# Kernel optimization log

Hardware: AMD Instinct MI355X
Metric: run time of the kernel (lower is better)

Reference implementation:

```python
import jax, jax.numpy as jnp
import numpy as np

N = 100000   # nodes
E = 1000000  # edges
F_IN = 128
H = 256
G = 64       # graphs in batch
EPS = 1e-5   # BatchNorm eps


def setup_inputs() -> dict:
    key = jax.random.key(0)
    ks = jax.random.split(key, 16)
    s = 0.05
    d = {}
    d["x"] = jax.random.normal(ks[0], (N, F_IN), jnp.float32)
    d["edge_index"] = jax.random.randint(ks[1], (2, E), 0, N, dtype=jnp.int32)
    d["batch"] = jnp.sort(jax.random.randint(ks[2], (N,), 0, G, dtype=jnp.int32))
    # block1 (128 -> 256, has projection)
    d["W1"] = jax.random.normal(ks[3], (F_IN, H), jnp.float32) * s
    d["b1"] = jnp.zeros((H,), jnp.float32)
    d["g1"] = jnp.ones((H,), jnp.float32)
    d["be1"] = jnp.zeros((H,), jnp.float32)
    d["P1"] = jax.random.normal(ks[4], (F_IN, H), jnp.float32) * s
    # blocks 2-4 (256 -> 256)
    for i, k in zip((2, 3, 4), (ks[5], ks[6], ks[7])):
        d[f"W{i}"] = jax.random.normal(k, (H, H), jnp.float32) * s
        d[f"b{i}"] = jnp.zeros((H,), jnp.float32)
        d[f"g{i}"] = jnp.ones((H,), jnp.float32)
        d[f"be{i}"] = jnp.zeros((H,), jnp.float32)
    d["Wl"] = jax.random.normal(ks[8], (H, 1), jnp.float32) * s
    d["bl"] = jnp.zeros((1,), jnp.float32)
    return d


def _gcn_norm(edge_index):
    # PyG gcn_norm: add self-loops, deg from dst column, norm = d^-1/2[src]*d^-1/2[dst]
    src, dst = edge_index[0], edge_index[1]
    deg = jax.ops.segment_sum(jnp.ones((E,), jnp.float32), dst, num_segments=N) + 1.0
    dis = jax.lax.rsqrt(deg)
    enorm = dis[src] * dis[dst]          # [E] normalization per edge
    self_w = 1.0 / deg                   # self-loop weight = deg^-1
    return src, dst, enorm, self_w


def _block(x, src, dst, enorm, self_w, W, b, g, be, P=None):
    hw = x @ W                                            # [N, H]
    msg = hw[src] * enorm[:, None]                        # [E, H] gather
    agg = jax.ops.segment_sum(msg, dst, num_segments=N)   # scatter-add
    agg = agg + hw * self_w[:, None] + b                  # self-loop + bias
    # BatchNorm1d (training-mode batch statistics, biased variance)
    m = jnp.mean(agg, axis=0)
    v = jnp.var(agg, axis=0)
    out = jax.nn.relu((agg - m) * jax.lax.rsqrt(v + EPS) * g + be)
    res = x @ P if P is not None else x
    return out + res


def reference(x, edge_index, batch, W1, b1, g1, be1, P1,
              W2, b2, g2, be2, W3, b3, g3, be3, W4, b4, g4, be4, Wl, bl):
    src, dst, enorm, self_w = _gcn_norm(edge_index)
    h = _block(x, src, dst, enorm, self_w, W1, b1, g1, be1, P1)
    h = _block(h, src, dst, enorm, self_w, W2, b2, g2, be2)
    h = _block(h, src, dst, enorm, self_w, W3, b3, g3, be3)
    h = _block(h, src, dst, enorm, self_w, W4, b4, g4, be4)
    # global mean pool over graphs
    sums = jax.ops.segment_sum(h, batch, num_segments=G)                       # [G, H]
    cnt = jax.ops.segment_sum(jnp.ones((N,), jnp.float32), batch, num_segments=G)
    pooled = sums / jnp.maximum(cnt, 1.0)[:, None]
    return pooled @ Wl + bl                                                    # [G, 1]
```

## Files before the change

### kernel.cpp

```cpp
#include <hip/hip_runtime.h>
#include <cstdint>
#include <cstddef>

#define NN 100000
#define NE 1000000
#define FIN 128
#define HD 256
#define NG 64
#define BNEPS 1e-5f

typedef unsigned short ushort_t;
typedef __attribute__((ext_vector_type(8))) short bf16x8;
typedef __attribute__((ext_vector_type(4))) float f32x4;


__device__ inline float b2f(unsigned short u) {
    union { float f; unsigned int i; } x; x.i = ((unsigned int)u) << 16; return x.f;
}
__device__ inline unsigned short f2b(float f) {
    union { float f; unsigned int i; } x; x.f = f;
    unsigned int r = x.i + 0x7FFFu + ((x.i >> 16) & 1u);
    return (unsigned short)(r >> 16);
}
__device__ inline float  ld1(const unsigned short* p) { return b2f(*p); }
__device__ inline float4 ld4v(const unsigned short* p) {
    ushort4 u = *(const ushort4*)p;
    return make_float4(b2f(u.x), b2f(u.y), b2f(u.z), b2f(u.w));
}
__device__ inline float2 ld2v(const unsigned short* p) {
    ushort2 u = *(const ushort2*)p;
    return make_float2(b2f(u.x), b2f(u.y));
}
__device__ inline void st4v(unsigned short* p, float4 v) {
    ushort4 u; u.x = f2b(v.x); u.y = f2b(v.y); u.z = f2b(v.z); u.w = f2b(v.w);
    *(ushort4*)p = u;
}
__device__ inline void st2v(unsigned short* p, float2 v) {
    ushort2 u; u.x = f2b(v.x); u.y = f2b(v.y);
    *(ushort2*)p = u;
}


__global__ __launch_bounds__(256) void count_deg_k(const int* __restrict__ dst, int* __restrict__ cnt) {
    int e = blockIdx.x * 256 + threadIdx.x;
    if (e < NE) atomicAdd(&cnt[dst[e]], 1);
}

__global__ __launch_bounds__(256) void node_prep_k(const int* __restrict__ cnt,
                                                   float* __restrict__ dis, float* __restrict__ selfw) {
    int i = blockIdx.x * 256 + threadIdx.x;
    if (i < NN) {
        float d = (float)cnt[i] + 1.0f;
        dis[i] = rsqrtf(d);
        selfw[i] = 1.0f / d;
    }
}

__global__ __launch_bounds__(1024) void scan_reduce_k(const int* __restrict__ cnt, int* __restrict__ partials) {
    __shared__ int sh[1024];
    int i = blockIdx.x * 1024 + threadIdx.x;
    sh[threadIdx.x] = (i < NN) ? cnt[i] : 0;
    __syncthreads();
    for (int off = 512; off > 0; off >>= 1) {
        if (threadIdx.x < off) sh[threadIdx.x] += sh[threadIdx.x + off];
        __syncthreads();
    }
    if (threadIdx.x == 0) partials[blockIdx.x] = sh[0];
}

__global__ void scan_partials_k(int* partials, int nb) {
    if (threadIdx.x == 0 && blockIdx.x == 0) {
        int run = 0;
        for (int b = 0; b < nb; b++) { int v = partials[b]; partials[b] = run; run += v; }
    }
}

__global__ __launch_bounds__(1024) void scan_write_k(const int* __restrict__ cnt,
                                                     const int* __restrict__ partials,
                                                     int* __restrict__ rowptr) {
    __shared__ int sh[1024];
    int i = blockIdx.x * 1024 + threadIdx.x;
    int v = (i < NN) ? cnt[i] : 0;
    sh[threadIdx.x] = v;
    __syncthreads();
    for (int off = 1; off < 1024; off <<= 1) {
        int t = (threadIdx.x >= off) ? sh[threadIdx.x - off] : 0;
        __syncthreads();
        sh[threadIdx.x] += t;
        __syncthreads();
    }
    if (i < NN) rowptr[i] = partials[blockIdx.x] + sh[threadIdx.x] - v;
    if (i == NN - 1) rowptr[NN] = partials[blockIdx.x] + sh[threadIdx.x];
}

__global__ __launch_bounds__(256) void fill_csr_k(const int* __restrict__ src, const int* __restrict__ dst,
                                                  const int* __restrict__ rowptr, int* __restrict__ cursor,
                                                  const float* __restrict__ dis,
                                                  int2* __restrict__ csr) {
    int e = blockIdx.x * 256 + threadIdx.x;
    if (e < NE) {
        int d = dst[e], s = src[e];
        int pos = rowptr[d] + atomicAdd(&cursor[d], 1);
        float w = dis[s] * dis[d];
        csr[pos] = make_int2(s, __float_as_int(w));
    }
}

__global__ __launch_bounds__(256) void x2b_k(const float* __restrict__ x, unsigned short* __restrict__ xb) {
    int i = blockIdx.x * 256 + threadIdx.x;
    if (i < NN * FIN / 4) {
        float4 v = *reinterpret_cast<const float4*>(x + (size_t)i * 4);
        ushort4 u; u.x = f2b(v.x); u.y = f2b(v.y); u.z = f2b(v.z); u.w = f2b(v.w);
        *reinterpret_cast<ushort4*>(xb + (size_t)i * 4) = u;
    }
}

__global__ __launch_bounds__(256) void wt_all_k(const float* __restrict__ W1, const float* __restrict__ P1,
                                                const float* __restrict__ W2, const float* __restrict__ W3,
                                                const float* __restrict__ W4,
                                                unsigned short* __restrict__ w1t, unsigned short* __restrict__ p1t,
                                                unsigned short* __restrict__ w2t, unsigned short* __restrict__ w3t,
                                                unsigned short* __restrict__ w4t) {
    int b = blockIdx.x;
    const float* W; unsigned short* Bt; int K; int base;
    if (b < 128)      { W = W1; Bt = w1t; K = 128; base = b; }
    else if (b < 256) { W = P1; Bt = p1t; K = 128; base = b - 128; }
    else if (b < 512) { W = W2; Bt = w2t; K = 256; base = b - 256; }
    else if (b < 768) { W = W3; Bt = w3t; K = 256; base = b - 512; }
    else              { W = W4; Bt = w4t; K = 256; base = b - 768; }
    int i = base * 256 + threadIdx.x;
    if (i < K * 256) {
        int k = i >> 8, n = i & 255;
        Bt[n * K + k] = f2b(W[k * 256 + n]);
    }
}


template<int COLS>
__global__ __launch_bounds__(256) void spmm_k(const unsigned short* __restrict__ h,
                                              const int* __restrict__ rowptr,
                                              const int2* __restrict__ csr,
                                              const float* __restrict__ selfw,
                                              unsigned short* __restrict__ z) {
    const int lane = threadIdx.x & 63;
    const int row = blockIdx.x * 4 + (threadIdx.x >> 6);
    if (row >= NN) return;
    if constexpr (COLS == 256) {
        float4 a = ld4v(h + (size_t)row * COLS + lane * 4);
        float sw = selfw[row];
        float4 acc = make_float4(a.x * sw, a.y * sw, a.z * sw, a.w * sw);
        int e = rowptr[row];
        const int e1 = rowptr[row + 1];
        for (; e + 8 <= e1; e += 8) {
            int2 cc[8];
#pragma unroll
            for (int j = 0; j < 8; j++) cc[j] = csr[e + j];
            float4 hv[8];
#pragma unroll
            for (int j = 0; j < 8; j++) hv[j] = ld4v(h + (size_t)cc[j].x * COLS + lane * 4);
#pragma unroll
            for (int j = 0; j < 8; j++) {
                float w = __int_as_float(cc[j].y);
                acc.x += w * hv[j].x; acc.y += w * hv[j].y; acc.z += w * hv[j].z; acc.w += w * hv[j].w;
            }
        }
        for (; e + 4 <= e1; e += 4) {
            int2 c0 = csr[e], c1 = csr[e + 1], c2 = csr[e + 2], c3 = csr[e + 3];
            float4 h0 = ld4v(h + (size_t)c0.x * COLS + lane * 4);
            float4 h1 = ld4v(h + (size_t)c1.x * COLS + lane * 4);
            float4 h2 = ld4v(h + (size_t)c2.x * COLS + lane * 4);
            float4 h3 = ld4v(h + (size_t)c3.x * COLS + lane * 4);
            float w0 = __int_as_float(c0.y), w1 = __int_as_float(c1.y);
            float w2 = __int_as_float(c2.y), w3 = __int_as_float(c3.y);
            acc.x += w0 * h0.x; acc.y += w0 * h0.y; acc.z += w0 * h0.z; acc.w += w0 * h0.w;
            acc.x += w1 * h1.x; acc.y += w1 * h1.y; acc.z += w1 * h1.z; acc.w += w1 * h1.w;
            acc.x += w2 * h2.x; acc.y += w2 * h2.y; acc.z += w2 * h2.z; acc.w += w2 * h2.w;
            acc.x += w3 * h3.x; acc.y += w3 * h3.y; acc.z += w3 * h3.z; acc.w += w3 * h3.w;
        }
        for (; e < e1; e++) {
            int2 c = csr[e];
            float w = __int_as_float(c.y);
            float4 hv = ld4v(h + (size_t)c.x * COLS + lane * 4);
            acc.x += w * hv.x; acc.y += w * hv.y; acc.z += w * hv.z; acc.w += w * hv.w;
        }
        st4v(z + (size_t)row * COLS + lane * 4, acc);
    } else {
        float2 a = ld2v(h + (size_t)row * COLS + lane * 2);
        float sw = selfw[row];
        float2 acc = make_float2(a.x * sw, a.y * sw);
        int e = rowptr[row];
        const int e1 = rowptr[row + 1];
        for (; e + 8 <= e1; e += 8) {
            int2 cc[8];
#pragma unroll
            for (int j = 0; j < 8; j++) cc[j] = csr[e + j];
            float2 hv[8];
#pragma unroll
            for (int j = 0; j < 8; j++) hv[j] = ld2v(h + (size_t)cc[j].x * COLS + lane * 2);
#pragma unroll
            for (int j = 0; j < 8; j++) {
                float w = __int_as_float(cc[j].y);
                acc.x += w * hv[j].x; acc.y += w * hv[j].y;
            }
        }
        for (; e + 4 <= e1; e += 4) {
            int2 c0 = csr[e], c1 = csr[e + 1], c2 = csr[e + 2], c3 = csr[e + 3];
            float2 h0 = ld2v(h + (size_t)c0.x * COLS + lane * 2);
            float2 h1 = ld2v(h + (size_t)c1.x * COLS + lane * 2);
            float2 h2 = ld2v(h + (size_t)c2.x * COLS + lane * 2);
            float2 h3 = ld2v(h + (size_t)c3.x * COLS + lane * 2);
            float w0 = __int_as_float(c0.y), w1 = __int_as_float(c1.y);
            float w2 = __int_as_float(c2.y), w3 = __int_as_float(c3.y);
            acc.x += w0 * h0.x; acc.y += w0 * h0.y;
            acc.x += w1 * h1.x; acc.y += w1 * h1.y;
            acc.x += w2 * h2.x; acc.y += w2 * h2.y;
            acc.x += w3 * h3.x; acc.y += w3 * h3.y;
        }
        for (; e < e1; e++) {
            int2 c = csr[e];
            float w = __int_as_float(c.y);
            float2 hv = ld2v(h + (size_t)c.x * COLS + lane * 2);
            acc.x += w * hv.x; acc.y += w * hv.y;
        }
        st2v(z + (size_t)row * COLS + lane * 2, acc);
    }
}


template<int K, int MODE>
__global__ __launch_bounds__(512) void mgemm_k(const unsigned short* __restrict__ A,
                                               const unsigned short* __restrict__ Bt,
                                               const float* __restrict__ bias,
                                               unsigned short* __restrict__ C,
                                               const float* __restrict__ scale,
                                               const float* __restrict__ shift,
                                               const unsigned short* __restrict__ aggin,
                                               float* __restrict__ sums, int M) {
    constexpr int NCOLS = 128;
    constexpr int NF = NCOLS / 16;
    constexpr int SEGS = K / 8;
    constexpr int KS = K / 32;
    __shared__ char Bl[NCOLS * K * 2];
    __shared__ float sstat[2 * NCOLS];
    const int tid  = threadIdx.x;
    const int lane = tid & 63;
    const int wid  = tid >> 6;
    const int q    = lane >> 4;
    const int rl   = lane & 15;
    const int col0 = blockIdx.y * NCOLS;
    const int row0 = blockIdx.x * 256 + wid * 32;

    for (int s = tid; s < NCOLS * SEGS; s += 512) {
        int col = s / SEGS, j = s % SEGS;
        uint4 v = *reinterpret_cast<const uint4*>(Bt + (size_t)(col0 + col) * K + j * 8);
        *reinterpret_cast<uint4*>(Bl + col * (K * 2) + (((j) ^ (col & 7)) << 4)) = v;
    }
    if (MODE == 0 && tid < 2 * NCOLS) sstat[tid] = 0.f;
    __syncthreads();

    const int a0r = min(row0 + rl, M - 1);
    const int a1r = min(row0 + 16 + rl, M - 1);
    const unsigned short* pa0 = A + (size_t)a0r * K + q * 8;
    const unsigned short* pa1 = A + (size_t)a1r * K + q * 8;
    bf16x8 af0[KS], af1[KS];
#pragma unroll
    for (int ks = 0; ks < KS; ks++) {
        af0[ks] = *reinterpret_cast<const bf16x8*>(pa0 + ks * 32);
        af1[ks] = *reinterpret_cast<const bf16x8*>(pa1 + ks * 32);
    }

    f32x4 acc[2][NF];
#pragma unroll
    for (int m = 0; m < 2; m++)
#pragma unroll
        for (int n = 0; n < NF; n++) acc[m][n] = (f32x4){0.f, 0.f, 0.f, 0.f};

#pragma unroll
    for (int ks = 0; ks < KS; ks++) {
#pragma unroll
        for (int nf = 0; nf < NF; nf++) {
            int col = nf * 16 + rl;
            bf16x8 bf = *reinterpret_cast<const bf16x8*>(Bl + col * (K * 2) + (((ks * 4 + q) ^ (col & 7)) << 4));
            acc[0][nf] = __builtin_amdgcn_mfma_f32_16x16x32_bf16(bf, af0[ks], acc[0][nf], 0, 0, 0);
            acc[1][nf] = __builtin_amdgcn_mfma_f32_16x16x32_bf16(bf, af1[ks], acc[1][nf], 0, 0, 0);
        }
    }

    const int g0 = row0 + rl, g1 = row0 + 16 + rl;
    const bool ok0 = g0 < M, ok1 = g1 < M;
#pragma unroll
    for (int nf = 0; nf < NF; nf++) {
        int cb = col0 + nf * 16 + q * 4;
        f32x4 v0 = acc[0][nf], v1 = acc[1][nf];
        if (MODE == 0) {
            float4 bb = *reinterpret_cast<const float4*>(bias + cb);
            v0[0] += bb.x; v0[1] += bb.y; v0[2] += bb.z; v0[3] += bb.w;
            v1[0] += bb.x; v1[1] += bb.y; v1[2] += bb.z; v1[3] += bb.w;
        } else {
            float4 sc = *reinterpret_cast<const float4*>(scale + cb);
            float4 sh = *reinterpret_cast<const float4*>(shift + cb);
            if (ok0) {
                ushort4 ag = *reinterpret_cast<const ushort4*>(aggin + (size_t)g0 * HD + cb);
                v0[0] += fmaxf(fmaf(b2f(ag.x), sc.x, sh.x), 0.f);
                v0[1] += fmaxf(fmaf(b2f(ag.y), sc.y, sh.y), 0.f);
                v0[2] += fmaxf(fmaf(b2f(ag.z), sc.z, sh.z), 0.f);
                v0[3] += fmaxf(fmaf(b2f(ag.w), sc.w, sh.w), 0.f);
            }
            if (ok1) {
                ushort4 ag = *reinterpret_cast<const ushort4*>(aggin + (size_t)g1 * HD + cb);
                v1[0] += fmaxf(fmaf(b2f(ag.x), sc.x, sh.x), 0.f);
                v1[1] += fmaxf(fmaf(b2f(ag.y), sc.y, sh.y), 0.f);
                v1[2] += fmaxf(fmaf(b2f(ag.z), sc.z, sh.z), 0.f);
                v1[3] += fmaxf(fmaf(b2f(ag.w), sc.w, sh.w), 0.f);
            }
        }
        if (ok0) {
            ushort4 u; u.x = f2b(v0[0]); u.y = f2b(v0[1]); u.z = f2b(v0[2]); u.w = f2b(v0[3]);
            *reinterpret_cast<ushort4*>(C + (size_t)g0 * HD + cb) = u;
        }
        if (ok1) {
            ushort4 u; u.x = f2b(v1[0]); u.y = f2b(v1[1]); u.z = f2b(v1[2]); u.w = f2b(v1[3]);
            *reinterpret_cast<ushort4*>(C + (size_t)g1 * HD + cb) = u;
        }
        if (MODE == 0) {
            if (!ok0) { v0[0] = v0[1] = v0[2] = v0[3] = 0.f; }
            if (!ok1) { v1[0] = v1[1] = v1[2] = v1[3] = 0.f; }
            float s[4], qq[4];
#pragma unroll
            for (int j = 0; j < 4; j++) {
                s[j]  = v0[j] + v1[j];
                qq[j] = v0[j] * v0[j] + v1[j] * v1[j];
            }
#pragma unroll
            for (int m = 1; m < 16; m <<= 1) {
#pragma unroll
                for (int j = 0; j < 4; j++) {
                    s[j]  += __shfl_xor(s[j], m, 64);
                    qq[j] += __shfl_xor(qq[j], m, 64);
                }
            }
            if (rl == 0) {
                int cl = nf * 16 + q * 4;
#pragma unroll
                for (int j = 0; j < 4; j++) {
                    atomicAdd(&sstat[cl + j], s[j]);
                    atomicAdd(&sstat[NCOLS + cl + j], qq[j]);
                }
            }
        }
    }

    if (MODE == 0) {
        __syncthreads();
        if (tid < NCOLS)            atomicAdd(&sums[col0 + tid], sstat[tid]);
        else if (tid < 2 * NCOLS)   atomicAdd(&sums[HD + col0 + (tid - NCOLS)], sstat[tid]);
    }
}


__global__ void bn_fin_k(const float* __restrict__ sums, const float* __restrict__ g,
                         const float* __restrict__ be, float* __restrict__ sc, float* __restrict__ sh) {
    int c = threadIdx.x;
    float m = sums[c] * (1.0f / NN);
    float v = sums[HD + c] * (1.0f / NN) - m * m;
    float s = g[c] * rsqrtf(v + BNEPS);
    sc[c] = s;
    sh[c] = be[c] - m * s;
}

__global__ __launch_bounds__(256) void epi_k(const unsigned short* __restrict__ agg,
                                             const unsigned short* __restrict__ res,
                                             const float* __restrict__ scp, const float* __restrict__ shp,
                                             unsigned short* __restrict__ out) {
    const size_t total = (size_t)NN * (HD / 4);
    size_t i = (size_t)blockIdx.x * 256 + threadIdx.x;
    const size_t stride = (size_t)gridDim.x * 256;
    for (; i < total; i += stride) {
        int cq = ((int)(i & 63)) * 4;
        float4 a = ld4v(agg + i * 4);
        float4 r = ld4v(res + i * 4);
        float4 sc = *reinterpret_cast<const float4*>(scp + cq);
        float4 sh = *reinterpret_cast<const float4*>(shp + cq);
        float4 o;
        o.x = fmaxf(fmaf(a.x, sc.x, sh.x), 0.f) + r.x;
        o.y = fmaxf(fmaf(a.y, sc.y, sh.y), 0.f) + r.y;
        o.z = fmaxf(fmaf(a.z, sc.z, sh.z), 0.f) + r.z;
        o.w = fmaxf(fmaf(a.w, sc.w, sh.w), 0.f) + r.w;
        st4v(out + i * 4, o);
    }
}


__global__ __launch_bounds__(256) void pool_sum_k(const unsigned short* __restrict__ h,
                                                  const int* __restrict__ batch,
                                                  float* __restrict__ pooled) {
    const int c = threadIdx.x;
    const int rs = blockIdx.x * 256;
    if (rs >= NN) return;
    const int re = min(rs + 256, NN);
    float acc = 0.f;
    int cur = batch[rs];
    for (int r = rs; r < re; r++) {
        int g = batch[r];
        if (g != cur) { atomicAdd(&pooled[(size_t)cur * HD + c], acc); acc = 0.f; cur = g; }
        acc += ld1(h + (size_t)r * HD + c);
    }
    atomicAdd(&pooled[(size_t)cur * HD + c], acc);
}

__global__ void pool_out_k(const float* __restrict__ pooled, const int* __restrict__ batch,
                           const float* __restrict__ Wl, const float* __restrict__ bl,
                           float* __restrict__ out) {
    int g = threadIdx.x;
    if (g < NG) {
        auto lb = [&](int val) {
            int lo = 0, hi = NN;
            while (lo < hi) { int mid = (lo + hi) >> 1; if (batch[mid] < val) lo = mid + 1; else hi = mid; }
            return lo;
        };
        int c0 = lb(g), c1 = lb(g + 1);
        float cn = fmaxf((float)(c1 - c0), 1.0f);
        float s = 0.f;
        for (int c = 0; c < HD; c++) s += pooled[(size_t)g * HD + c] * Wl[c];
        out[g] = s / cn + bl[0];
    }
}


static inline size_t alignup(size_t x) { return (x + 255) & ~size_t(255); }

extern "C" void kernel_launch(void* const* d_in, const int* in_sizes, int n_in,
                              void* d_out, int out_size, void* d_ws, size_t ws_size,
                              hipStream_t stream) {
    const float* x    = (const float*)d_in[0];
    const int*   ei   = (const int*)d_in[1];
    const int*   bat  = (const int*)d_in[2];
    const float* W1   = (const float*)d_in[3];
    const float* bi1  = (const float*)d_in[4];
    const float* g1   = (const float*)d_in[5];
    const float* be1  = (const float*)d_in[6];
    const float* P1   = (const float*)d_in[7];
    const float* W2   = (const float*)d_in[8];
    const float* bi2  = (const float*)d_in[9];
    const float* g2   = (const float*)d_in[10];
    const float* be2  = (const float*)d_in[11];
    const float* W3   = (const float*)d_in[12];
    const float* bi3  = (const float*)d_in[13];
    const float* g3   = (const float*)d_in[14];
    const float* be3  = (const float*)d_in[15];
    const float* W4   = (const float*)d_in[16];
    const float* bi4  = (const float*)d_in[17];
    const float* g4   = (const float*)d_in[18];
    const float* be4  = (const float*)d_in[19];
    const float* Wl   = (const float*)d_in[20];
    const float* bl   = (const float*)d_in[21];
    float* out = (float*)d_out;

    const int* e_src = ei;
    const int* e_dst = ei + NE;

    typedef unsigned short ST;
    char* p = (char*)d_ws;
    auto alloc = [&](size_t bytes) { char* q = p; p += alignup(bytes); return q; };
    ST*    fb0     = (ST*)alloc((size_t)NN * HD * sizeof(ST));
    ST*    fb1     = (ST*)alloc((size_t)NN * HD * sizeof(ST));
    ST*    fb2     = (ST*)alloc((size_t)NN * HD * sizeof(ST));
    ST*    xb      = (ST*)alloc((size_t)NN * FIN * sizeof(ST));
    float* dis     = (float*)alloc((size_t)NN * 4);
    float* selfw   = (float*)alloc((size_t)NN * 4);
    int*   rowptr  = (int*)alloc((size_t)(NN + 1) * 4);
    int2*  csr     = (int2*)alloc((size_t)NE * 8);
    int*   partials= (int*)alloc(128 * 4);
    float* bnsc    = (float*)alloc(HD * 4);
    float* bnsh    = (float*)alloc(HD * 4);
    ST*    w1t     = (ST*)alloc(256 * 128 * sizeof(ST));
    ST*    p1t     = (ST*)alloc(256 * 128 * sizeof(ST));
    ST*    w2t     = (ST*)alloc(256 * 256 * sizeof(ST));
    ST*    w3t     = (ST*)alloc(256 * 256 * sizeof(ST));
    ST*    w4t     = (ST*)alloc(256 * 256 * sizeof(ST));
    size_t zbytes = (size_t)NN * 4 + (size_t)NN * 4 + 4 * 2 * HD * 4 + (size_t)NG * HD * 4;
    char*  zbase   = alloc(zbytes);
    int*   cnt     = (int*)zbase;
    int*   cursor  = (int*)(zbase + (size_t)NN * 4);
    float* sums1   = (float*)(zbase + (size_t)NN * 8);
    float* sums2   = sums1 + 2 * HD;
    float* sums3   = sums2 + 2 * HD;
    float* sums4   = sums3 + 2 * HD;
    float* pooled  = sums4 + 2 * HD;

    const int NB = (NN + 1023) / 1024;
    dim3 gg((NN + 255) / 256, 2);

    hipMemsetAsync(zbase, 0, zbytes, stream);

    wt_all_k<<<1024, 256, 0, stream>>>(W1, P1, W2, W3, W4, w1t, p1t, w2t, w3t, w4t);
    x2b_k<<<(NN * FIN / 4 + 255) / 256, 256, 0, stream>>>(x, xb);

    count_deg_k<<<(NE + 255) / 256, 256, 0, stream>>>(e_dst, cnt);
    node_prep_k<<<(NN + 255) / 256, 256, 0, stream>>>(cnt, dis, selfw);
    scan_reduce_k<<<NB, 1024, 0, stream>>>(cnt, partials);
    scan_partials_k<<<1, 64, 0, stream>>>(partials, NB);
    scan_write_k<<<NB, 1024, 0, stream>>>(cnt, partials, rowptr);
    fill_csr_k<<<(NE + 255) / 256, 256, 0, stream>>>(e_src, e_dst, rowptr, cursor, dis, csr);

    spmm_k<128><<<NN / 4, 256, 0, stream>>>(xb, rowptr, csr, selfw, fb0);
    mgemm_k<128, 0><<<gg, 512, 0, stream>>>(fb0, w1t, bi1, fb2, nullptr, nullptr, nullptr, sums1, NN);
    bn_fin_k<<<1, 256, 0, stream>>>(sums1, g1, be1, bnsc, bnsh);
    mgemm_k<128, 1><<<gg, 512, 0, stream>>>(xb, p1t, nullptr, fb1, bnsc, bnsh, fb2, nullptr, NN);

    spmm_k<256><<<NN / 4, 256, 0, stream>>>(fb1, rowptr, csr, selfw, fb0);
    mgemm_k<256, 0><<<gg, 512, 0, stream>>>(fb0, w2t, bi2, fb2, nullptr, nullptr, nullptr, sums2, NN);
    bn_fin_k<<<1, 256, 0, stream>>>(sums2, g2, be2, bnsc, bnsh);
    epi_k<<<4096, 256, 0, stream>>>(fb2, fb1, bnsc, bnsh, fb0);

    spmm_k<256><<<NN / 4, 256, 0, stream>>>(fb0, rowptr, csr, selfw, fb1);
    mgemm_k<256, 0><<<gg, 512, 0, stream>>>(fb1, w3t, bi3, fb2, nullptr, nullptr, nullptr, sums3, NN);
    bn_fin_k<<<1, 256, 0, stream>>>(sums3, g3, be3, bnsc, bnsh);
    epi_k<<<4096, 256, 0, stream>>>(fb2, fb0, bnsc, bnsh, fb1);

    spmm_k<256><<<NN / 4, 256, 0, stream>>>(fb1, rowptr, csr, selfw, fb0);
    mgemm_k<256, 0><<<gg, 512, 0, stream>>>(fb0, w4t, bi4, fb2, nullptr, nullptr, nullptr, sums4, NN);
    bn_fin_k<<<1, 256, 0, stream>>>(sums4, g4, be4, bnsc, bnsh);
    epi_k<<<4096, 256, 0, stream>>>(fb2, fb1, bnsc, bnsh, fb0);

    pool_sum_k<<<(NN + 255) / 256, 256, 0, stream>>>(fb0, bat, pooled);
    pool_out_k<<<1, 64, 0, stream>>>(pooled, bat, Wl, bl, out);
}
```

Before: 846.9 us.

## Make GEMM persistent over row chunks and fuse final epilogue into pooling

The GEMM grid shrinks to 256x2 blocks, each covering 391 rows in two 256-row passes. This amortises the shared-memory B-tile load and the per-block stat atomics over more rows. A-fragments are now loaded per k-step instead of preloaded, and launch_bounds adds a min-blocks hint to cut register pressure. The last block's BN/ReLU/residual epilogue is folded into the pooling kernel, which removes one full write and read of the N×H activation. Risks are less latency hiding from the per-k A loads and uneven tail work across blocks.

Result: faster. 798.8 us (-5.7%).

```diff
diff --git a/kernel.cpp b/kernel.cpp
--- a/kernel.cpp
+++ b/kernel.cpp
@@ -227,15 +227,17 @@
 }
 
 
+#define RPB 391
+
 template<int K, int MODE>
-__global__ __launch_bounds__(512) void mgemm_k(const unsigned short* __restrict__ A,
-                                               const unsigned short* __restrict__ Bt,
-                                               const float* __restrict__ bias,
-                                               unsigned short* __restrict__ C,
-                                               const float* __restrict__ scale,
-                                               const float* __restrict__ shift,
-                                               const unsigned short* __restrict__ aggin,
-                                               float* __restrict__ sums, int M) {
+__global__ __launch_bounds__(512, 4) void mgemm_k(const unsigned short* __restrict__ A,
+                                                  const unsigned short* __restrict__ Bt,
+                                                  const float* __restrict__ bias,
+                                                  unsigned short* __restrict__ C,
+                                                  const float* __restrict__ scale,
+                                                  const float* __restrict__ shift,
+                                                  const unsigned short* __restrict__ aggin,
+                                                  float* __restrict__ sums, int M) {
     constexpr int NCOLS = 128;
     constexpr int NF = NCOLS / 16;
     constexpr int SEGS = K / 8;
@@ -248,7 +250,8 @@
     const int q    = lane >> 4;
     const int rl   = lane & 15;
     const int col0 = blockIdx.y * NCOLS;
-    const int row0 = blockIdx.x * 256 + wid * 32;
+    const int rbase = blockIdx.x * RPB;
+    const int rend  = min(rbase + RPB, M);
 
     for (int s = tid; s < NCOLS * SEGS; s += 512) {
         int col = s / SEGS, j = s % SEGS;
@@ -258,93 +261,94 @@
     if (MODE == 0 && tid < 2 * NCOLS) sstat[tid] = 0.f;
     __syncthreads();
 
-    const int a0r = min(row0 + rl, M - 1);
-    const int a1r = min(row0 + 16 + rl, M - 1);
-    const unsigned short* pa0 = A + (size_t)a0r * K + q * 8;
-    const unsigned short* pa1 = A + (size_t)a1r * K + q * 8;
-    bf16x8 af0[KS], af1[KS];
-#pragma unroll
-    for (int ks = 0; ks < KS; ks++) {
-        af0[ks] = *reinterpret_cast<const bf16x8*>(pa0 + ks * 32);
-        af1[ks] = *reinterpret_cast<const bf16x8*>(pa1 + ks * 32);
-    }
-
-    f32x4 acc[2][NF];
-#pragma unroll
-    for (int m = 0; m < 2; m++)
-#pragma unroll
-        for (int n = 0; n < NF; n++) acc[m][n] = (f32x4){0.f, 0.f, 0.f, 0.f};
-
-#pragma unroll
-    for (int ks = 0; ks < KS; ks++) {
+    for (int it = 0; it < 2; it++) {
+        const int row0 = rbase + it * 256 + wid * 32;
+        if (row0 >= rend) continue;
+
+        const int a0r = min(row0 + rl, M - 1);
+        const int a1r = min(row0 + 16 + rl, M - 1);
+        const unsigned short* pa0 = A + (size_t)a0r * K + q * 8;
+        const unsigned short* pa1 = A + (size_t)a1r * K + q * 8;
+
+        f32x4 acc[2][NF];
+#pragma unroll
+        for (int m = 0; m < 2; m++)
+#pragma unroll
+            for (int n = 0; n < NF; n++) acc[m][n] = (f32x4){0.f, 0.f, 0.f, 0.f};
+
+#pragma unroll
+        for (int ks = 0; ks < KS; ks++) {
+            bf16x8 af0 = *reinterpret_cast<const bf16x8*>(pa0 + ks * 32);
+            bf16x8 af1 = *reinterpret_cast<const bf16x8*>(pa1 + ks * 32);
+#pragma unroll
+            for (int nf = 0; nf < NF; nf++) {
+                int col = nf * 16 + rl;
+                bf16x8 bf = *reinterpret_cast<const bf16x8*>(Bl + col * (K * 2) + (((ks * 4 + q) ^ (col & 7)) << 4));
+                acc[0][nf] = __builtin_amdgcn_mfma_f32_16x16x32_bf16(bf, af0, acc[0][nf], 0, 0, 0);
+                acc[1][nf] = __builtin_amdgcn_mfma_f32_16x16x32_bf16(bf, af1, acc[1][nf], 0, 0, 0);
+            }
+        }
+
+        const int g0 = row0 + rl, g1 = row0 + 16 + rl;
+        const bool ok0 = g0 < rend, ok1 = g1 < rend;
 #pragma unroll
         for (int nf = 0; nf < NF; nf++) {
-            int col = nf * 16 + rl;
-            bf16x8 bf = *reinterpret_cast<const bf16x8*>(Bl + col * (K * 2) + (((ks * 4 + q) ^ (col & 7)) << 4));
-            acc[0][nf] = __builtin_amdgcn_mfma_f32_16x16x32_bf16(bf, af0[ks], acc[0][nf], 0, 0, 0);
-            acc[1][nf] = __builtin_amdgcn_mfma_f32_16x16x32_bf16(bf, af1[ks], acc[1][nf], 0, 0, 0);
-        }
-    }
-
-    const int g0 = row0 + rl, g1 = row0 + 16 + rl;
-    const bool ok0 = g0 < M, ok1 = g1 < M;
-#pragma unroll
-    for (int nf = 0; nf < NF; nf++) {
-        int cb = col0 + nf * 16 + q * 4;
-        f32x4 v0 = acc[0][nf], v1 = acc[1][nf];
-        if (MODE == 0) {
-            float4 bb = *reinterpret_cast<const float4*>(bias + cb);
-            v0[0] += bb.x; v0[1] += bb.y; v0[2] += bb.z; v0[3] += bb.w;
-            v1[0] += bb.x; v1[1] += bb.y; v1[2] += bb.z; v1[3] += bb.w;
-        } else {
-            float4 sc = *reinterpret_cast<const float4*>(scale + cb);
-            float4 sh = *reinterpret_cast<const float4*>(shift + cb);
+            int cb = col0 + nf * 16 + q * 4;
+            f32x4 v0 = acc[0][nf], v1 = acc[1][nf];
+            if (MODE == 0) {
+                float4 bb = *reinterpret_cast<const float4*>(bias + cb);
+                v0[0] += bb.x; v0[1] += bb.y; v0[2] += bb.z; v0[3] += bb.w;
+                v1[0] += bb.x; v1[1] += bb.y; v1[2] += bb.z; v1[3] += bb.w;
+            } else {
+                float4 sc = *reinterpret_cast<const float4*>(scale + cb);
+                float4 sh = *reinterpret_cast<const float4*>(shift + cb);
+                if (ok0) {
+                    ushort4 ag = *reinterpret_cast<const ushort4*>(aggin + (size_t)g0 * HD + cb);
+                    v0[0] += fmaxf(fmaf(b2f(ag.x), sc.x, sh.x), 0.f);
+                    v0[1] += fmaxf(fmaf(b2f(ag.y), sc.y, sh.y), 0.f);
+                    v0[2] += fmaxf(fmaf(b2f(ag.z), sc.z, sh.z), 0.f);
+                    v0[3] += fmaxf(fmaf(b2f(ag.w), sc.w, sh.w), 0.f);
+                }
+                if (ok1) {
+                    ushort4 ag = *reinterpret_cast<const ushort4*>(aggin + (size_t)g1 * HD + cb);
+                    v1[0] += fmaxf(fmaf(b2f(ag.x), sc.x, sh.x), 0.f);
+                    v1[1] += fmaxf(fmaf(b2f(ag.y), sc.y, sh.y), 0.f);
+                    v1[2] += fmaxf(fmaf(b2f(ag.z), sc.z, sh.z), 0.f);
+                    v1[3] += fmaxf(fmaf(b2f(ag.w), sc.w, sh.w), 0.f);
+                }
+            }
             if (ok0) {
-                ushort4 ag = *reinterpret_cast<const ushort4*>(aggin + (size_t)g0 * HD + cb);
-                v0[0] += fmaxf(fmaf(b2f(ag.x), sc.x, sh.x), 0.f);
-                v0[1] += fmaxf(fmaf(b2f(ag.y), sc.y, sh.y), 0.f);
-                v0[2] += fmaxf(fmaf(b2f(ag.z), sc.z, sh.z), 0.f);
-                v0[3] += fmaxf(fmaf(b2f(ag.w), sc.w, sh.w), 0.f);
+                ushort4 u; u.x = f2b(v0[0]); u.y = f2b(v0[1]); u.z = f2b(v0[2]); u.w = f2b(v0[3]);
+                *reinterpret_cast<ushort4*>(C + (size_t)g0 * HD + cb) = u;
             }
             if (ok1) {
-                ushort4 ag = *reinterpret_cast<const ushort4*>(aggin + (size_t)g1 * HD + cb);
-                v1[0] += fmaxf(fmaf(b2f(ag.x), sc.x, sh.x), 0.f);
-                v1[1] += fmaxf(fmaf(b2f(ag.y), sc.y, sh.y), 0.f);
-                v1[2] += fmaxf(fmaf(b2f(ag.z), sc.z, sh.z), 0.f);
-                v1[3] += fmaxf(fmaf(b2f(ag.w), sc.w, sh.w), 0.f);
-            }
-        }
-        if (ok0) {
-            ushort4 u; u.x = f2b(v0[0]); u.y = f2b(v0[1]); u.z = f2b(v0[2]); u.w = f2b(v0[3]);
-            *reinterpret_cast<ushort4*>(C + (size_t)g0 * HD + cb) = u;
-        }
-        if (ok1) {
-            ushort4 u; u.x = f2b(v1[0]); u.y = f2b(v1[1]); u.z = f2b(v1[2]); u.w = f2b(v1[3]);
-            *reinterpret_cast<ushort4*>(C + (size_t)g1 * HD + cb) = u;
-        }
-        if (MODE == 0) {
-            if (!ok0) { v0[0] = v0[1] = v0[2] = v0[3] = 0.f; }
-            if (!ok1) { v1[0] = v1[1] = v1[2] = v1[3] = 0.f; }
-            float s[4], qq[4];
-#pragma unroll
-            for (int j = 0; j < 4; j++) {
-                s[j]  = v0[j] + v1[j];
-                qq[j] = v0[j] * v0[j] + v1[j] * v1[j];
-            }
-#pragma unroll
-            for (int m = 1; m < 16; m <<= 1) {
+                ushort4 u; u.x = f2b(v1[0]); u.y = f2b(v1[1]); u.z = f2b(v1[2]); u.w = f2b(v1[3]);
+                *reinterpret_cast<ushort4*>(C + (size_t)g1 * HD + cb) = u;
+            }
+            if (MODE == 0) {
+                if (!ok0) { v0[0] = v0[1] = v0[2] = v0[3] = 0.f; }
+                if (!ok1) { v1[0] = v1[1] = v1[2] = v1[3] = 0.f; }
+                float s[4], qq[4];
 #pragma unroll
                 for (int j = 0; j < 4; j++) {
-                    s[j]  += __shfl_xor(s[j], m, 64);
-                    qq[j] += __shfl_xor(qq[j], m, 64);
+                    s[j]  = v0[j] + v1[j];
+                    qq[j] = v0[j] * v0[j] + v1[j] * v1[j];
                 }
-            }
-            if (rl == 0) {
-                int cl = nf * 16 + q * 4;
-#pragma unroll
-                for (int j = 0; j < 4; j++) {
-                    atomicAdd(&sstat[cl + j], s[j]);
-                    atomicAdd(&sstat[NCOLS + cl + j], qq[j]);
+#pragma unroll
+                for (int m = 1; m < 16; m <<= 1) {
+#pragma unroll
+                    for (int j = 0; j < 4; j++) {
+                        s[j]  += __shfl_xor(s[j], m, 64);
+                        qq[j] += __shfl_xor(qq[j], m, 64);
+                    }
+                }
+                if (rl == 0) {
+                    int cl = nf * 16 + q * 4;
+#pragma unroll
+                    for (int j = 0; j < 4; j++) {
+                        atomicAdd(&sstat[cl + j], s[j]);
+                        atomicAdd(&sstat[NCOLS + cl + j], qq[j]);
+                    }
                 }
             }
         }
@@ -391,19 +395,24 @@
 }
 
 
-__global__ __launch_bounds__(256) void pool_sum_k(const unsigned short* __restrict__ h,
+__global__ __launch_bounds__(256) void epi_pool_k(const unsigned short* __restrict__ lin,
+                                                  const unsigned short* __restrict__ res,
+                                                  const float* __restrict__ scp, const float* __restrict__ shp,
                                                   const int* __restrict__ batch,
                                                   float* __restrict__ pooled) {
     const int c = threadIdx.x;
-    const int rs = blockIdx.x * 256;
+    const int rs = blockIdx.x * 250;
     if (rs >= NN) return;
-    const int re = min(rs + 256, NN);
+    const int re = min(rs + 250, NN);
+    const float sc = scp[c], sh = shp[c];
     float acc = 0.f;
     int cur = batch[rs];
     for (int r = rs; r < re; r++) {
         int g = batch[r];
         if (g != cur) { atomicAdd(&pooled[(size_t)cur * HD + c], acc); acc = 0.f; cur = g; }
-        acc += ld1(h + (size_t)r * HD + c);
+        float a = b2f(lin[(size_t)r * HD + c]);
+        float rr = b2f(res[(size_t)r * HD + c]);
+        acc += fmaxf(fmaf(a, sc, sh), 0.f) + rr;
     }
     atomicAdd(&pooled[(size_t)cur * HD + c], acc);
 }
@@ -489,7 +498,7 @@
     float* pooled  = sums4 + 2 * HD;
 
     const int NB = (NN + 1023) / 1024;
-    dim3 gg((NN + 255) / 256, 2);
+    dim3 gg(256, 2);
 
     hipMemsetAsync(zbase, 0, zbytes, stream);
 
@@ -521,8 +530,6 @@
     spmm_k<256><<<NN / 4, 256, 0, stream>>>(fb1, rowptr, csr, selfw, fb0);
     mgemm_k<256, 0><<<gg, 512, 0, stream>>>(fb0, w4t, bi4, fb2, nullptr, nullptr, nullptr, sums4, NN);
     bn_fin_k<<<1, 256, 0, stream>>>(sums4, g4, be4, bnsc, bnsh);
-    epi_k<<<4096, 256, 0, stream>>>(fb2, fb1, bnsc, bnsh, fb0);
-
-    pool_sum_k<<<(NN + 255) / 256, 256, 0, stream>>>(fb0, bat, pooled);
+    epi_pool_k<<<(NN + 249) / 250, 256, 0, stream>>>(fb2, fb1, bnsc, bnsh, bat, pooled);
     pool_out_k<<<1, 64, 0, stream>>>(pooled, bat, Wl, bl, out);
 }
```
